# Performance work log

Hardware: AMD Instinct MI355X
Metric: run time of the kernel (lower is better)

## Reference

```python
import jax, jax.numpy as jnp
import numpy as np

NUM_QUBITS = 15
DEPTH = 3
BATCH = 512
DIM = 2 ** NUM_QUBITS


def _apply_1q_batched(state, gate, q, n):
    # state: [B, 2^n] complex64, gate: [B, 2, 2] complex64, qubit q (little-endian)
    B = state.shape[0]
    L, R = 2 ** (n - 1 - q), 2 ** q
    s = state.reshape(B, L, 2, R)
    return jnp.einsum('bij,bljr->blir', gate, s).reshape(B, -1)


def _apply_1q_shared(state, gate, q, n):
    # gate: [2, 2] shared across batch
    B = state.shape[0]
    L, R = 2 ** (n - 1 - q), 2 ** q
    s = state.reshape(B, L, 2, R)
    return jnp.einsum('ij,bljr->blir', gate, s).reshape(B, -1)


def _apply_cz(state, q, n):
    # CZ on adjacent qubits (q, q+1): sign flip on |..11..>
    B = state.shape[0]
    L, R = 2 ** (n - 2 - q), 2 ** q
    s = state.reshape(B, L, 2, 2, R)
    phase = jnp.array([[1.0, 1.0], [1.0, -1.0]], dtype=state.dtype)
    return (s * phase[None, None, :, :, None]).reshape(B, -1)


def _simulate(state_batch, theta, n, depth):
    B = state_batch.shape[0]
    cdtype = jnp.complex64
    state = jnp.zeros((B, 2 ** n), dtype=cdtype).at[:, 0].set(1.0)
    # RX encoding layer: per-sample angles x_q on wire q
    for q in range(n):
        half = 0.5 * state_batch[:, q]
        c = jnp.cos(half).astype(cdtype)
        s = jnp.sin(half).astype(cdtype)
        gate = jnp.stack([jnp.stack([c, -1j * s], axis=-1),
                          jnp.stack([-1j * s, c], axis=-1)], axis=-2)  # [B,2,2]
        state = _apply_1q_batched(state, gate, q, n)
    # Variational layers: RY(theta) per wire, then CZ chain
    idx = 0
    for _ in range(depth):
        for q in range(n):
            half = 0.5 * theta[idx]
            idx += 1
            c = jnp.cos(half).astype(cdtype)
            s = jnp.sin(half).astype(cdtype)
            gate = jnp.stack([jnp.stack([c, -s]), jnp.stack([s, c])])  # [2,2]
            state = _apply_1q_shared(state, gate, q, n)
        for q in range(n - 1):
            state = _apply_cz(state, q, n)
    return state


def _z_signs(n):
    # signs[k, q] = +1 if bit q of basis index k is 0 else -1
    idx = jnp.arange(2 ** n, dtype=jnp.int32)
    bits = (idx[:, None] >> jnp.arange(n, dtype=jnp.int32)[None, :]) & 1
    return (1.0 - 2.0 * bits).astype(jnp.float32)  # [2^n, n]


def setup_inputs() -> dict:
    key = jax.random.key(0)
    k1, k2, k3, k4 = jax.random.split(key, 4)
    state_batch = jax.random.normal(k1, (BATCH, NUM_QUBITS), dtype=jnp.float32)
    theta = jax.random.normal(k2, (NUM_QUBITS * DEPTH,), dtype=jnp.float32)
    bound = 1.0 / np.sqrt(NUM_QUBITS)
    head_w = jax.random.uniform(k3, (1, NUM_QUBITS), jnp.float32, -bound, bound)
    head_b = jax.random.uniform(k4, (1,), jnp.float32, -bound, bound)
    return {"state_batch": state_batch, "theta": theta, "head_w": head_w, "head_b": head_b}


def reference(state_batch, theta, head_w, head_b):
    n = NUM_QUBITS
    state = _simulate(state_batch, theta, n, DEPTH)  # [B, 2^n] complex64
    probs = state.real ** 2 + state.imag ** 2        # [B, 2^n] float32
    zq = probs @ _z_signs(n)                         # [B, n], col q = <Z_q>
    # qiskit Pauli string 'I'*j + 'Z' + ...: output col j is Z on qubit n-1-j
    expect = zq[:, ::-1]
    out = expect @ head_w.T + head_b                 # [B, 1]
    return out.squeeze(-1)
```

## Files before the change

kernel.cpp:

```cpp
#include <hip/hip_runtime.h>

#define NQ 15

template<int T>
__device__ inline void apply_ry(float (&re)[32], float (&im)[32], float cg, float sg) {
#pragma unroll
    for (int x = 0; x < 32; x++) {
        if (!(x & (1 << T))) {
            const int y = x | (1 << T);
            float r0 = re[x], i0 = im[x], r1 = re[y], i1 = im[y];
            re[x] = cg * r0 - sg * r1;
            im[x] = cg * i0 - sg * i1;
            re[y] = sg * r0 + cg * r1;
            im[y] = sg * i0 + cg * i1;
        }
    }
}

__global__ __launch_bounds__(256)
void HybridRegression_lightcone2_kernel(const float* __restrict__ sb,
                                        const float* __restrict__ theta,
                                        const float* __restrict__ hw,
                                        const float* __restrict__ hb,
                                        float* __restrict__ out,
                                        int batch) {
    const int wave = threadIdx.x >> 6;
    const int lane = threadIdx.x & 63;
    int b = blockIdx.x * 4 + wave;
    const bool bv = (b < batch);
    if (!bv) b = batch - 1;

    const int q = lane;
    const bool qv = (q < NQ);

    const float a  = qv ? sb[b * NQ + q]    : 0.0f;
    const float t1 = qv ? theta[q]          : 0.0f;
    const float t2 = qv ? theta[NQ + q]     : 0.0f;
    const float t3 = qv ? theta[2 * NQ + q] : 0.0f;

    float sh, ch;  sincosf(0.5f * a,  &sh, &ch);
    float s1, c1;  sincosf(0.5f * t1, &s1, &c1);
    float s2, c2;  sincosf(0.5f * t2, &s2, &c2);
    float s3, c3;  sincosf(t3,        &s3, &c3);

    const float x0 = c1 * ch, y0 = s1 * sh;
    const float x1 = s1 * ch, y1 = -c1 * sh;

    float fx0[5], fy0[5], fx1[5], fy1[5];
#pragma unroll
    for (int w = 0; w < 5; w++) {
        const int j = q - 2 + w;
        const int src = (j >= 0 && j < NQ) ? j : NQ;
        fx0[w] = __shfl(x0, src, 64);
        fy0[w] = __shfl(y0, src, 64);
        fx1[w] = __shfl(x1, src, 64);
        fy1[w] = __shfl(y1, src, 64);
    }
    float g2c[3], g2s[3];
#pragma unroll
    for (int w = 0; w < 3; w++) {
        const int j = q - 1 + w;
        const int src = (j >= 0 && j < NQ) ? j : NQ;
        g2c[w] = __shfl(c2, src, 64);
        g2s[w] = __shfl(s2, src, 64);
    }

    float re[32], im[32];
    re[0] = fx0[0]; im[0] = fy0[0];
    re[1] = fx1[0]; im[1] = fy1[0];
#pragma unroll
    for (int w = 1; w < 5; w++) {
#pragma unroll
        for (int x = 0; x < 16; x++) {
            if (x < (1 << w)) {
                const int y = x + (1 << w);
                const float r = re[x], i = im[x];
                re[y] = r * fx1[w] - i * fy1[w];
                im[y] = r * fy1[w] + i * fx1[w];
                re[x] = r * fx0[w] - i * fy0[w];
                im[x] = r * fy0[w] + i * fx0[w];
            }
        }
    }

#pragma unroll
    for (int x = 0; x < 32; x++) {
        const int p = (((x >> 0) & 3) == 3) + (((x >> 1) & 3) == 3)
                    + (((x >> 2) & 3) == 3) + (((x >> 3) & 3) == 3);
        if (p & 1) { re[x] = -re[x]; im[x] = -im[x]; }
    }

    apply_ry<1>(re, im, g2c[0], g2s[0]);
    apply_ry<2>(re, im, g2c[1], g2s[1]);
    apply_ry<3>(re, im, g2c[2], g2s[2]);

#pragma unroll
    for (int x = 0; x < 32; x++) {
        const int p = (((x >> 1) & 3) == 3) + (((x >> 2) & 3) == 3);
        if (p & 1) { re[x] = -re[x]; im[x] = -im[x]; }
    }

    float zd = 0.0f, zc = 0.0f;
#pragma unroll
    for (int x = 0; x < 32; x++) {
        if (!(x & 4)) {
            const int y = x | 4;
            zd += (re[x] * re[x] + im[x] * im[x]) - (re[y] * re[y] + im[y] * im[y]);
            zc += re[x] * re[y] + im[x] * im[y];
        }
    }
    const float zq = c3 * zd - 2.0f * s3 * zc;

    float contrib = qv ? hw[(NQ - 1) - q] * zq : 0.0f;

#pragma unroll
    for (int off = 32; off >= 1; off >>= 1)
        contrib += __shfl_xor(contrib, off, 64);

    if (lane == 0 && bv)
        out[b] = contrib + hb[0];
}

extern "C" void kernel_launch(void* const* d_in, const int* in_sizes, int n_in,
                              void* d_out, int out_size, void* d_ws, size_t ws_size,
                              hipStream_t stream) {
    const float* sb    = (const float*)d_in[0];
    const float* theta = (const float*)d_in[1];
    const float* hw    = (const float*)d_in[2];
    const float* hb    = (const float*)d_in[3];
    float* out = (float*)d_out;

    const int batch = in_sizes[0] / NQ;
    const int blocks = (batch + 3) / 4;

    hipLaunchKernelGGL(HybridRegression_lightcone2_kernel,
                       dim3(blocks), dim3(256), 0, stream,
                       sb, theta, hw, hb, out, batch);
}
```

Before: 61.22 us.

## Split each qubit's 5-qubit lightcone state across two lanes, two samples per wave

Each wave now handles two batch samples, and each qubit's 32-amplitude lightcone state is split across two lanes. Each lane holds 16 amplitudes, with the top lightcone qubit fixed by the lane's half index. This halves per-lane register and arithmetic work and packs more useful lanes into each wave, since only 15 of 64 lanes did useful work before. The cost is a shorter shuffle reduction, extra lane-index arithmetic, and a per-half sign flip. The Z-expectation sum over the fixed bit comes from adding the two half-lanes in the reduction.

```diff
diff --git a/kernel.cpp b/kernel.cpp
--- a/kernel.cpp
+++ b/kernel.cpp
@@ -3,9 +3,9 @@
 #define NQ 15
 
 template<int T>
-__device__ inline void apply_ry(float (&re)[32], float (&im)[32], float cg, float sg) {
+__device__ inline void apply_ry16(float (&re)[16], float (&im)[16], float cg, float sg) {
 #pragma unroll
-    for (int x = 0; x < 32; x++) {
+    for (int x = 0; x < 16; x++) {
         if (!(x & (1 << T))) {
             const int y = x | (1 << T);
             float r0 = re[x], i0 = im[x], r1 = re[y], i1 = im[y];
@@ -18,7 +18,7 @@
 }
 
 __global__ __launch_bounds__(256)
-void HybridRegression_lightcone2_kernel(const float* __restrict__ sb,
+void HybridRegression_lightcone3_kernel(const float* __restrict__ sb,
                                         const float* __restrict__ theta,
                                         const float* __restrict__ hw,
                                         const float* __restrict__ hb,
@@ -26,11 +26,13 @@
                                         int batch) {
     const int wave = threadIdx.x >> 6;
     const int lane = threadIdx.x & 63;
-    int b = blockIdx.x * 4 + wave;
+    const int e = lane >> 5;
+    const int h = (lane >> 4) & 1;
+    const int q = lane & 15;
+
+    int b = blockIdx.x * 8 + wave * 2 + e;
     const bool bv = (b < batch);
     if (!bv) b = batch - 1;
-
-    const int q = lane;
     const bool qv = (q < NQ);
 
     const float a  = qv ? sb[b * NQ + q]    : 0.0f;
@@ -46,11 +48,12 @@
     const float x0 = c1 * ch, y0 = s1 * sh;
     const float x1 = s1 * ch, y1 = -c1 * sh;
 
+    const int grp = lane & 48;
     float fx0[5], fy0[5], fx1[5], fy1[5];
 #pragma unroll
     for (int w = 0; w < 5; w++) {
         const int j = q - 2 + w;
-        const int src = (j >= 0 && j < NQ) ? j : NQ;
+        const int src = grp | ((j >= 0 && j < NQ) ? j : NQ);
         fx0[w] = __shfl(x0, src, 64);
         fy0[w] = __shfl(y0, src, 64);
         fx1[w] = __shfl(x1, src, 64);
@@ -60,18 +63,18 @@
 #pragma unroll
     for (int w = 0; w < 3; w++) {
         const int j = q - 1 + w;
-        const int src = (j >= 0 && j < NQ) ? j : NQ;
+        const int src = grp | ((j >= 0 && j < NQ) ? j : NQ);
         g2c[w] = __shfl(c2, src, 64);
         g2s[w] = __shfl(s2, src, 64);
     }
 
-    float re[32], im[32];
+    float re[16], im[16];
     re[0] = fx0[0]; im[0] = fy0[0];
     re[1] = fx1[0]; im[1] = fy1[0];
 #pragma unroll
-    for (int w = 1; w < 5; w++) {
+    for (int w = 1; w < 4; w++) {
 #pragma unroll
-        for (int x = 0; x < 16; x++) {
+        for (int x = 0; x < 8; x++) {
             if (x < (1 << w)) {
                 const int y = x + (1 << w);
                 const float r = re[x], i = im[x];
@@ -82,42 +85,52 @@
             }
         }
     }
+    const float gx = h ? fx1[4] : fx0[4];
+    const float gy = h ? fy1[4] : fy0[4];
+#pragma unroll
+    for (int x = 0; x < 16; x++) {
+        const float r = re[x], i = im[x];
+        re[x] = r * gx - i * gy;
+        im[x] = r * gy + i * gx;
+    }
 
 #pragma unroll
-    for (int x = 0; x < 32; x++) {
+    for (int x = 0; x < 16; x++) {
         const int p = (((x >> 0) & 3) == 3) + (((x >> 1) & 3) == 3)
-                    + (((x >> 2) & 3) == 3) + (((x >> 3) & 3) == 3);
+                    + (((x >> 2) & 3) == 3);
         if (p & 1) { re[x] = -re[x]; im[x] = -im[x]; }
     }
+    if (h) {
+#pragma unroll
+        for (int x = 8; x < 16; x++) { re[x] = -re[x]; im[x] = -im[x]; }
+    }
 
-    apply_ry<1>(re, im, g2c[0], g2s[0]);
-    apply_ry<2>(re, im, g2c[1], g2s[1]);
-    apply_ry<3>(re, im, g2c[2], g2s[2]);
+    apply_ry16<1>(re, im, g2c[0], g2s[0]);
+    apply_ry16<2>(re, im, g2c[1], g2s[1]);
+    apply_ry16<3>(re, im, g2c[2], g2s[2]);
 
 #pragma unroll
-    for (int x = 0; x < 32; x++) {
+    for (int x = 0; x < 16; x++) {
         const int p = (((x >> 1) & 3) == 3) + (((x >> 2) & 3) == 3);
         if (p & 1) { re[x] = -re[x]; im[x] = -im[x]; }
     }
 
     float zd = 0.0f, zc = 0.0f;
 #pragma unroll
-    for (int x = 0; x < 32; x++) {
+    for (int x = 0; x < 16; x++) {
         if (!(x & 4)) {
             const int y = x | 4;
             zd += (re[x] * re[x] + im[x] * im[x]) - (re[y] * re[y] + im[y] * im[y]);
             zc += re[x] * re[y] + im[x] * im[y];
         }
     }
-    const float zq = c3 * zd - 2.0f * s3 * zc;
-
-    float contrib = qv ? hw[(NQ - 1) - q] * zq : 0.0f;
+    float contrib = qv ? hw[(NQ - 1) - q] * (c3 * zd - 2.0f * s3 * zc) : 0.0f;
 
 #pragma unroll
-    for (int off = 32; off >= 1; off >>= 1)
+    for (int off = 16; off >= 1; off >>= 1)
         contrib += __shfl_xor(contrib, off, 64);
 
-    if (lane == 0 && bv)
+    if ((lane & 31) == 0 && bv)
         out[b] = contrib + hb[0];
 }
 
@@ -131,9 +144,9 @@
     float* out = (float*)d_out;
 
     const int batch = in_sizes[0] / NQ;
-    const int blocks = (batch + 3) / 4;
+    const int blocks = (batch + 7) / 8;
 
-    hipLaunchKernelGGL(HybridRegression_lightcone2_kernel,
+    hipLaunchKernelGGL(HybridRegression_lightcone3_kernel,
                        dim3(blocks), dim3(256), 0, stream,
                        sb, theta, hw, hb, out, batch);
 }
```

Result: no change. 60.84 us (-0.6%).
